# Kernel optimization log

Hardware: AMD Instinct MI355X
Metric: run time of the kernel (lower is better)

## Reference

```python
import jax, jax.numpy as jnp
import numpy as np

BETA = 100.0
# (in_ch, out_ch) for the 12 effective 1x1-conv layers. ResNeXt blocks are
# fused: all branches read the same block input, so stacking branch weights
# along out-channels gives one GEMM per block.
LAYER_DIMS = [(259, 515), (515, 512), (512, 512), (512, 576), (576, 576),
              (576, 768), (768, 768), (768, 768), (768, 960), (960, 960),
              (960, 896), (896, 1)]


def setup_inputs() -> dict:
    key = jax.random.key(0)
    keys = jax.random.split(key, 2 + len(LAYER_DIMS))
    B, N = 2, 8192
    inp = {
        "input": jax.random.normal(keys[0], (B, N, 3), dtype=jnp.float32),
        "latent": jax.random.normal(keys[1], (B, 256), dtype=jnp.float32),
    }
    for i, (cin, cout) in enumerate(LAYER_DIMS):
        std = np.sqrt(2.0) / np.sqrt(cin)
        inp[f"W{i+1}"] = std * jax.random.normal(keys[2 + i], (cout, cin), dtype=jnp.float32)
        inp[f"b{i+1}"] = jnp.zeros((cout,), dtype=jnp.float32)
    return inp


def _sp(z):
    # torch Softplus(beta=100): softplus(beta*z)/beta (jax.nn.softplus is stable)
    return jax.nn.softplus(BETA * z) / BETA


def reference(input, latent,
              W1, b1, W2, b2, W3, b3, W4, b4, W5, b5, W6, b6,
              W7, b7, W8, b8, W9, b9, W10, b10, W11, b11, W12, b12):
    B, N, _ = input.shape
    lat = jnp.broadcast_to(latent[:, None, :], (B, N, latent.shape[-1]))
    x = jnp.concatenate([input, lat], axis=-1)  # (B, N, 259)
    input_con = x

    # layer 1: conv + softplus, grad seeded from first 3 input columns (xyz)
    z = x @ W1.T + b1                                   # (B, N, 515)
    g = jax.nn.sigmoid(BETA * z)[..., None] * W1[:, :3]  # (B, N, 515, 3)
    x = _sp(z)

    mids = [(W2, b2), (W3, b3), (W4, b4), (W5, b5), (W6, b6), (W7, b7),
            (W8, b8), (W9, b9), (W10, b10), (W11, b11)]
    for W, b in mids:  # fixed small layer loop (10 fused ResNeXt blocks)
        z = x @ W.T + b                                 # (B, N, Cout)
        g = jax.nn.sigmoid(BETA * z)[..., None] * jnp.einsum('oc,bnci->bnoi', W, g)
        x = _sp(z)

    # final 1x1 conv, no activation
    z = x @ W12.T + b12                                 # (B, N, 1)
    g = jnp.einsum('oc,bnci->bnoi', W12, g)             # (B, N, 1, 3)
    # torch returns conv output channel-first: (B, 1, N)
    return (z.transpose(0, 2, 1), g, input_con)
```

## Files before the change

kernel.cpp:

```cpp
#include <hip/hip_runtime.h>
#include <math.h>


typedef unsigned short u16;
typedef _Float16 f16;
typedef f16   f16x8  __attribute__((ext_vector_type(8)));
typedef float f32x16 __attribute__((ext_vector_type(16)));

__device__ __forceinline__ u16   f2h(float x){ return __builtin_bit_cast(u16, (f16)x); }
__device__ __forceinline__ float h2f(u16 b){ return (float)__builtin_bit_cast(f16, b); }

__device__ __forceinline__ void glld16(const void* g, void* l){
  __builtin_amdgcn_global_load_lds(
      (const __attribute__((address_space(1))) unsigned*)g,
      (__attribute__((address_space(3))) unsigned*)l, 16, 0, 0);
}

template<int N> __device__ __forceinline__ void wait_vmcnt(){
  static_assert(N == 0 || N == 6 || N == 9, "unsupported vmcnt literal");
  if constexpr (N == 0) asm volatile("s_waitcnt vmcnt(0)" ::: "memory");
  if constexpr (N == 6) asm volatile("s_waitcnt vmcnt(6)" ::: "memory");
  if constexpr (N == 9) asm volatile("s_waitcnt vmcnt(9)" ::: "memory");
}

template<int NP>
__global__ __launch_bounds__(256, 2)
void fused_layer(const u16* __restrict__ Sin, long long psIn, int kpad,
                 u16* __restrict__ Sout, long long psOut, int opitch,
                 const u16* __restrict__ Wh, const u16* __restrict__ Wl,
                 const float* __restrict__ bias, const float* __restrict__ Wfirst,
                 int cout, int cinFirst)
{
  constexpr bool FIRST = (NP == 2);
  constexpr int  S     = NP + 4;
  __shared__ u16 As[2][NP][4][64][8];
  __shared__ u16 Bs[2][2][4][128][8];

  int bx = blockIdx.x, by = blockIdx.y;
  {
    const int gx = gridDim.x, gy = gridDim.y;
    const int nwg = gx * gy;
    const int d   = by * gx + bx;
    if ((nwg & 7) == 0){
      const int q = nwg >> 3;
      const int t = (d & 7) * q + (d >> 3);
      by = t % gy;
      bx = t / gy;
    }
  }

  const int tid   = threadIdx.x;
  const int w     = tid >> 6;
  const int lane  = tid & 63;
  const int lrow  = lane & 31;
  const int lhalf = lane >> 5;
  const int mh    = w >> 1;
  const int oh    = w & 1;
  const int m0    = bx * 64;
  const int o0    = by * 128;

  f32x16 zinit = {};
  f32x16 accx[2];
  f32x16 accg[FIRST ? 1 : 3][2];
  accx[0] = zinit; accx[1] = zinit;
  if constexpr (!FIRST){
    #pragma unroll
    for (int j = 0; j < 3; ++j){ accg[j][0] = zinit; accg[j][1] = zinit; }
  }

  const u16* aSrc[NP];
  #pragma unroll
  for (int p = 0; p < NP; ++p)
    aSrc[p] = Sin + (long long)p * psIn + (long long)(m0 + lane) * kpad + w * 8;
  const u16* bSrc[2][2];
  #pragma unroll
  for (int h = 0; h < 2; ++h){
    const u16* Wx = h ? Wl : Wh;
    #pragma unroll
    for (int hf = 0; hf < 2; ++hf)
      bSrc[h][hf] = Wx + (long long)(o0 + hf*64 + lane) * kpad + w * 8;
  }

  auto stage = [&](int buf, int kElem){
    #pragma unroll
    for (int p = 0; p < NP; ++p)
      glld16(aSrc[p] + kElem, &As[buf][p][w][0][0]);
    #pragma unroll
    for (int h = 0; h < 2; ++h)
      #pragma unroll
      for (int hf = 0; hf < 2; ++hf)
        glld16(bSrc[h][hf] + kElem, &Bs[buf][h][w][hf*64][0]);
  };

  auto compute = [&](int buf){
    __builtin_amdgcn_s_setprio(1);
    #pragma unroll
    for (int s = 0; s < 2; ++s){
      const int kq = s*2 + lhalf;
      f16x8 a[NP];
      #pragma unroll
      for (int p = 0; p < NP; ++p)
        a[p] = *(const f16x8*)&As[buf][p][kq][mh*32 + lrow][0];
      #pragma unroll
      for (int f = 0; f < 2; ++f){
        const int oc = oh*64 + f*32 + lrow;
        f16x8 bh = *(const f16x8*)&Bs[buf][0][kq][oc][0];
        f16x8 bl = *(const f16x8*)&Bs[buf][1][kq][oc][0];
        accx[f] = __builtin_amdgcn_mfma_f32_32x32x16_f16(a[0], bh, accx[f], 0,0,0);
        accx[f] = __builtin_amdgcn_mfma_f32_32x32x16_f16(a[1], bh, accx[f], 0,0,0);
        accx[f] = __builtin_amdgcn_mfma_f32_32x32x16_f16(a[0], bl, accx[f], 0,0,0);
        if constexpr (!FIRST){
          #pragma unroll
          for (int j = 0; j < 3; ++j)
            accg[j][f] = __builtin_amdgcn_mfma_f32_32x32x16_f16(a[2+j], bh, accg[j][f], 0,0,0);
        }
      }
    }
    __builtin_amdgcn_s_setprio(0);
  };

  const int nk = kpad >> 5;
  stage(0, 0);
  stage(1, 32);
  int cur = 0;
  for (int t = 0; t < nk - 1; ++t){
    wait_vmcnt<S>();
    __builtin_amdgcn_s_barrier();
    compute(cur);
    asm volatile("s_waitcnt lgkmcnt(0)" ::: "memory");
    __builtin_amdgcn_s_barrier();
    if (t + 2 < nk) stage(cur, (t + 2) * 32);
    cur ^= 1;
  }
  wait_vmcnt<0>();
  __builtin_amdgcn_s_barrier();
  compute(cur);

  const int mb = m0 + mh*32;
  #pragma unroll
  for (int f = 0; f < 2; ++f){
    const int o = o0 + oh*64 + f*32 + lrow;
    const float bo = (o < cout) ? bias[o] : 0.f;
    float w0 = 0.f, w1 = 0.f, w2 = 0.f;
    if constexpr (FIRST){
      if (o < cout){
        w0 = Wfirst[(long long)o*cinFirst + 0];
        w1 = Wfirst[(long long)o*cinFirst + 1];
        w2 = Wfirst[(long long)o*cinFirst + 2];
      }
    }
    #pragma unroll
    for (int r = 0; r < 16; ++r){
      const int m = mb + (r & 3) + ((r >> 2) << 3) + (lhalf << 2);
      const float z    = accx[f][r] + bo;
      const float gate = 1.f / (1.f + expf(-100.f * z));
      const float sp   = fmaxf(z, 0.f) + 0.01f * log1pf(expf(-100.f * fabsf(z)));
      const long long idx = (long long)m * opitch + o;
      const u16 xh = f2h(sp);
      Sout[idx]          = xh;
      Sout[psOut + idx]  = f2h(sp - h2f(xh));
      if constexpr (FIRST){
        Sout[2*psOut + idx] = f2h(gate * w0);
        Sout[3*psOut + idx] = f2h(gate * w1);
        Sout[4*psOut + idx] = f2h(gate * w2);
      } else {
        Sout[2*psOut + idx] = f2h(gate * accg[0][f][r]);
        Sout[3*psOut + idx] = f2h(gate * accg[1][f][r]);
        Sout[4*psOut + idx] = f2h(gate * accg[2][f][r]);
      }
    }
  }
}

__global__ __launch_bounds__(256)
void final_layer(const u16* __restrict__ Sin, long long ps, int kpad,
                 const float* __restrict__ W, const float* __restrict__ bias,
                 float* __restrict__ out1, float* __restrict__ out2,
                 int cin, int mBase)
{
  const int lane = threadIdx.x & 63;
  const int wv   = threadIdx.x >> 6;
  const int m = blockIdx.x * 4 + wv;
  const u16* row = Sin + (long long)m * kpad;
  float s0=0.f, s1=0.f, s2=0.f, s3=0.f;
  for (int c = lane; c < cin; c += 64){
    const float w = W[c];
    s0 += (h2f(row[c]) + h2f(row[ps + c])) * w;
    s1 += h2f(row[2*ps + c]) * w;
    s2 += h2f(row[3*ps + c]) * w;
    s3 += h2f(row[4*ps + c]) * w;
  }
  #pragma unroll
  for (int off = 32; off > 0; off >>= 1){
    s0 += __shfl_xor(s0, off); s1 += __shfl_xor(s1, off);
    s2 += __shfl_xor(s2, off); s3 += __shfl_xor(s3, off);
  }
  if (lane == 0){
    out1[mBase + m] = s0 + bias[0];
    float* g = out2 + (long long)(mBase + m) * 3;
    g[0] = s1; g[1] = s2; g[2] = s3;
  }
}

__global__ void prep_input(const float* __restrict__ input,
                           const float* __restrict__ latent,
                           float* __restrict__ out3,
                           u16* __restrict__ x0, long long psX0, int N)
{
  const int m = blockIdx.x;
  const int b = m / N;
  const int c = threadIdx.x;
  if (c >= 288) return;
  float v = 0.f;
  if (c < 3) v = input[(long long)m*3 + c];
  else if (c < 259) v = latent[(long long)b*256 + (c - 3)];
  if (c < 259) out3[(long long)m*259 + c] = v;
  const u16 h = f2h(v);
  x0[(long long)m*288 + c]        = h;
  x0[psX0 + (long long)m*288 + c] = f2h(v - h2f(h));
}

__global__ void split_w(const float* __restrict__ W, u16* __restrict__ wh,
                        u16* __restrict__ wl, int cout, int cin, int kpad, int total)
{
  const int idx = blockIdx.x * 256 + threadIdx.x;
  if (idx >= total) return;
  const int o = idx / kpad, c = idx % kpad;
  const float v = (o < cout && c < cin) ? W[(long long)o*cin + c] : 0.f;
  const u16 h = f2h(v);
  wh[idx] = h;
  wl[idx] = f2h(v - h2f(h));
}

extern "C" void kernel_launch(void* const* d_in, const int* in_sizes, int n_in,
                              void* d_out, int out_size, void* d_ws, size_t ws_size,
                              hipStream_t stream)
{
  static const int CIN [12] = {259,515,512,512,576,576,768,768,768,960,960,896};
  static const int COUT[12] = {515,512,512,576,576,768,768,768,960,960,896,1};
  int OPAD[11], KPAD[12];
  KPAD[0] = 288;
  for (int i = 0; i < 11; ++i){
    OPAD[i] = ((COUT[i] + 127) / 128) * 128;
    KPAD[i+1] = OPAD[i];
  }

  const float* input  = (const float*)d_in[0];
  const float* latent = (const float*)d_in[1];
  auto Wp = [&](int i){ return (const float*)d_in[2 + 2*i]; };
  auto Bp = [&](int i){ return (const float*)d_in[3 + 2*i]; };

  const int Bn = in_sizes[1] / 256;
  const int Nn = in_sizes[0] / (3 * Bn);
  const int M  = Bn * Nn;

  float* out1 = (float*)d_out;
  float* out2 = out1 + M;
  float* out3 = out2 + (size_t)M * 3;

  char* wsp = (char*)d_ws;
  u16 *WH[11], *WL[11];
  for (int i = 0; i < 11; ++i){
    const size_t sz = (size_t)OPAD[i] * KPAD[i] * 2;
    WH[i] = (u16*)wsp; wsp += sz;
    WL[i] = (u16*)wsp; wsp += sz;
  }
  u16* x0 = (u16*)wsp;
  const long long psX0 = (long long)M * 288;
  wsp += (size_t)2 * psX0 * 2;

  const size_t used = (size_t)(wsp - (char*)d_ws);
  const size_t remain = (ws_size > used) ? (ws_size - used) : 0;
  const size_t perPoint = (size_t)2 * 5 * 1024 * 2;
  long long pc = (long long)(remain / perPoint);
  pc &= ~63LL;
  int Pc = (int)((pc < 8192LL) ? pc : 8192LL);
  if (Pc > M) Pc = M;
  if (Pc < 64) Pc = 64;
  u16* bufA = (u16*)wsp;
  u16* bufB = bufA + (size_t)5 * Pc * 1024;

  prep_input<<<M, 320, 0, stream>>>(input, latent, out3, x0, psX0, Nn);
  for (int i = 0; i < 11; ++i){
    const int total = OPAD[i] * KPAD[i];
    split_w<<<(total + 255)/256, 256, 0, stream>>>(
        Wp(i), WH[i], WL[i], COUT[i], CIN[i], KPAD[i], total);
  }

  for (int cm0 = 0; cm0 < M; cm0 += Pc){
    const int Mc = (M - cm0 < Pc) ? (M - cm0) : Pc;

    {
      dim3 g(Mc/64, OPAD[0]/128);
      fused_layer<2><<<g, 256, 0, stream>>>(
          x0 + (long long)cm0 * 288, psX0, 288,
          bufA, (long long)Pc * OPAD[0], OPAD[0],
          WH[0], WL[0], Bp(0), Wp(0), COUT[0], CIN[0]);
    }
    u16* src = bufA;
    u16* dst = bufB;
    for (int i = 1; i <= 10; ++i){
      dim3 g(Mc/64, OPAD[i]/128);
      fused_layer<5><<<g, 256, 0, stream>>>(
          src, (long long)Pc * KPAD[i], KPAD[i],
          dst, (long long)Pc * OPAD[i], OPAD[i],
          WH[i], WL[i], Bp(i), nullptr, COUT[i], 0);
      u16* t = src; src = dst; dst = t;
    }
    final_layer<<<Mc/4, 256, 0, stream>>>(
        src, (long long)Pc * KPAD[11], KPAD[11],
        Wp(11), Bp(11), out1, out2, CIN[11], cm0);
  }
}
```

Measured before the change: 2.569 ms.

## Widen GEMM tile to 256 output channels with 8 waves and triple-buffered LDS

Each fused layer block now covers 64 points by 256 output channels using 512 threads (8 waves), so each staged A tile is reused across twice as many outputs. The load pipeline goes from double to triple buffering, with global->LDS chunks distributed evenly across waves and vmcnt waits computed per wave. Output channels are padded to 256, so some waves sit idle on layers whose width isn't a multiple of 256 (e.g. 515, 576, 896), and the larger LDS footprint may lower occupancy.

```diff
diff --git a/kernel.cpp b/kernel.cpp
--- a/kernel.cpp
+++ b/kernel.cpp
@@ -17,14 +17,18 @@
 }
 
 template<int N> __device__ __forceinline__ void wait_vmcnt(){
-  static_assert(N == 0 || N == 6 || N == 9, "unsupported vmcnt literal");
-  if constexpr (N == 0) asm volatile("s_waitcnt vmcnt(0)" ::: "memory");
-  if constexpr (N == 6) asm volatile("s_waitcnt vmcnt(6)" ::: "memory");
-  if constexpr (N == 9) asm volatile("s_waitcnt vmcnt(9)" ::: "memory");
+  static_assert(N==0||N==5||N==6||N==7||N==10||N==12||N==14, "bad vmcnt");
+  if constexpr (N == 0)  asm volatile("s_waitcnt vmcnt(0)"  ::: "memory");
+  if constexpr (N == 5)  asm volatile("s_waitcnt vmcnt(5)"  ::: "memory");
+  if constexpr (N == 6)  asm volatile("s_waitcnt vmcnt(6)"  ::: "memory");
+  if constexpr (N == 7)  asm volatile("s_waitcnt vmcnt(7)"  ::: "memory");
+  if constexpr (N == 10) asm volatile("s_waitcnt vmcnt(10)" ::: "memory");
+  if constexpr (N == 12) asm volatile("s_waitcnt vmcnt(12)" ::: "memory");
+  if constexpr (N == 14) asm volatile("s_waitcnt vmcnt(14)" ::: "memory");
 }
 
 template<int NP>
-__global__ __launch_bounds__(256, 2)
+__global__ __launch_bounds__(512, 2)
 void fused_layer(const u16* __restrict__ Sin, long long psIn, int kpad,
                  u16* __restrict__ Sout, long long psOut, int opitch,
                  const u16* __restrict__ Wh, const u16* __restrict__ Wl,
@@ -32,9 +36,15 @@
                  int cout, int cinFirst)
 {
   constexpr bool FIRST = (NP == 2);
-  constexpr int  S     = NP + 4;
-  __shared__ u16 As[2][NP][4][64][8];
-  __shared__ u16 Bs[2][2][4][128][8];
+  constexpr int ACH   = NP * 4;
+  constexpr int CH    = ACH + 32;
+  constexpr int ABUFE = NP * 2048;
+  constexpr int BUFE  = ABUFE + 16384;
+  constexpr int CBASE = CH / 8;
+  constexpr int CREM  = CH % 8;
+  constexpr int MAXC  = CBASE + (CREM ? 1 : 0);
+
+  __shared__ __align__(16) u16 lds[3 * BUFE];
 
   int bx = blockIdx.x, by = blockIdx.y;
   {
@@ -49,15 +59,37 @@
     }
   }
 
-  const int tid   = threadIdx.x;
-  const int w     = tid >> 6;
-  const int lane  = tid & 63;
-  const int lrow  = lane & 31;
-  const int lhalf = lane >> 5;
-  const int mh    = w >> 1;
-  const int oh    = w & 1;
-  const int m0    = bx * 64;
-  const int o0    = by * 128;
+  const int tid  = threadIdx.x;
+  const int ws   = __builtin_amdgcn_readfirstlane(tid >> 6);
+  const int lane = tid & 63;
+  const int lrow = lane & 31;
+  const int lhalf= lane >> 5;
+  const int mh   = ws & 1;
+  const int oq   = ws >> 1;
+  const int m0   = bx * 64;
+  const int o0   = by * 256;
+  const bool act = (o0 + oq * 64) < opitch;
+
+  const int cnt = (CREM && ws < CREM) ? CBASE + 1 : CBASE;
+  const int c0  = (CREM && ws < CREM) ? ws * (CBASE + 1)
+                                      : CREM * (CBASE + 1) + (ws - CREM) * CBASE;
+  const u16* gptr[MAXC];
+  int ldsOffE[MAXC];
+  #pragma unroll
+  for (int j = 0; j < MAXC; ++j){
+    const int c = c0 + ((j < cnt) ? j : 0);
+    if (c < ACH){
+      const int p = c >> 2, kq = c & 3;
+      gptr[j]    = Sin + (long long)p * psIn + (long long)m0 * kpad + kq * 8;
+      ldsOffE[j] = p * 2048 + kq * 512;
+    } else {
+      const int b = c - ACH;
+      const int h = b >> 4, kq = (b >> 2) & 3, gg = b & 3;
+      gptr[j]    = (h ? Wl : Wh) + (long long)(o0 + gg * 64) * kpad + kq * 8;
+      ldsOffE[j] = ABUFE + h * 8192 + kq * 2048 + gg * 512;
+    }
+  }
+  const int vLane = lane * kpad;
 
   f32x16 zinit = {};
   f32x16 accx[2];
@@ -68,44 +100,30 @@
     for (int j = 0; j < 3; ++j){ accg[j][0] = zinit; accg[j][1] = zinit; }
   }
 
-  const u16* aSrc[NP];
-  #pragma unroll
-  for (int p = 0; p < NP; ++p)
-    aSrc[p] = Sin + (long long)p * psIn + (long long)(m0 + lane) * kpad + w * 8;
-  const u16* bSrc[2][2];
-  #pragma unroll
-  for (int h = 0; h < 2; ++h){
-    const u16* Wx = h ? Wl : Wh;
+  auto stage = [&](int bufE, int ktE){
     #pragma unroll
-    for (int hf = 0; hf < 2; ++hf)
-      bSrc[h][hf] = Wx + (long long)(o0 + hf*64 + lane) * kpad + w * 8;
-  }
-
-  auto stage = [&](int buf, int kElem){
-    #pragma unroll
-    for (int p = 0; p < NP; ++p)
-      glld16(aSrc[p] + kElem, &As[buf][p][w][0][0]);
-    #pragma unroll
-    for (int h = 0; h < 2; ++h)
-      #pragma unroll
-      for (int hf = 0; hf < 2; ++hf)
-        glld16(bSrc[h][hf] + kElem, &Bs[buf][h][w][hf*64][0]);
+    for (int j = 0; j < MAXC; ++j)
+      if (j < cnt)
+        glld16(gptr[j] + vLane + ktE, &lds[bufE + ldsOffE[j]]);
   };
 
-  auto compute = [&](int buf){
+  auto compute = [&](int bufE){
+    if (!act) return;
     __builtin_amdgcn_s_setprio(1);
     #pragma unroll
     for (int s = 0; s < 2; ++s){
-      const int kq = s*2 + lhalf;
+      const int kq = s * 2 + lhalf;
+      const int aoff = bufE + kq * 512 + (mh * 32 + lrow) * 8;
       f16x8 a[NP];
       #pragma unroll
       for (int p = 0; p < NP; ++p)
-        a[p] = *(const f16x8*)&As[buf][p][kq][mh*32 + lrow][0];
+        a[p] = *(const f16x8*)&lds[aoff + p * 2048];
       #pragma unroll
       for (int f = 0; f < 2; ++f){
-        const int oc = oh*64 + f*32 + lrow;
-        f16x8 bh = *(const f16x8*)&Bs[buf][0][kq][oc][0];
-        f16x8 bl = *(const f16x8*)&Bs[buf][1][kq][oc][0];
+        const int row  = oq * 64 + f * 32 + lrow;
+        const int boff = bufE + ABUFE + kq * 2048 + row * 8;
+        f16x8 bh = *(const f16x8*)&lds[boff];
+        f16x8 bl = *(const f16x8*)&lds[boff + 8192];
         accx[f] = __builtin_amdgcn_mfma_f32_32x32x16_f16(a[0], bh, accx[f], 0,0,0);
         accx[f] = __builtin_amdgcn_mfma_f32_32x32x16_f16(a[1], bh, accx[f], 0,0,0);
         accx[f] = __builtin_amdgcn_mfma_f32_32x32x16_f16(a[0], bl, accx[f], 0,0,0);
@@ -121,32 +139,40 @@
 
   const int nk = kpad >> 5;
   stage(0, 0);
-  stage(1, 32);
-  int cur = 0;
-  for (int t = 0; t < nk - 1; ++t){
-    wait_vmcnt<S>();
+  stage(BUFE, 32);
+  stage(2 * BUFE, 64);
+  int bufE = 0;
+  for (int t = 0; t < nk; ++t){
+    const int ahead = nk - 1 - t;
+    if (ahead >= 2){
+      if (CREM && cnt == CBASE + 1) wait_vmcnt<2*CBASE + 2>();
+      else                          wait_vmcnt<2*CBASE>();
+    } else if (ahead == 1){
+      if (CREM && cnt == CBASE + 1) wait_vmcnt<CBASE + 1>();
+      else                          wait_vmcnt<CBASE>();
+    } else {
+      wait_vmcnt<0>();
+    }
     __builtin_amdgcn_s_barrier();
-    compute(cur);
+    compute(bufE);
     asm volatile("s_waitcnt lgkmcnt(0)" ::: "memory");
     __builtin_amdgcn_s_barrier();
-    if (t + 2 < nk) stage(cur, (t + 2) * 32);
-    cur ^= 1;
-  }
-  wait_vmcnt<0>();
-  __builtin_amdgcn_s_barrier();
-  compute(cur);
-
-  const int mb = m0 + mh*32;
+    if (t + 3 < nk) stage(bufE, (t + 3) * 32);
+    bufE += BUFE; if (bufE == 3 * BUFE) bufE = 0;
+  }
+
+  if (!act) return;
+  const int mb = m0 + mh * 32;
   #pragma unroll
   for (int f = 0; f < 2; ++f){
-    const int o = o0 + oh*64 + f*32 + lrow;
+    const int o = o0 + oq * 64 + f * 32 + lrow;
     const float bo = (o < cout) ? bias[o] : 0.f;
     float w0 = 0.f, w1 = 0.f, w2 = 0.f;
     if constexpr (FIRST){
       if (o < cout){
-        w0 = Wfirst[(long long)o*cinFirst + 0];
-        w1 = Wfirst[(long long)o*cinFirst + 1];
-        w2 = Wfirst[(long long)o*cinFirst + 2];
+        w0 = Wfirst[(long long)o * cinFirst + 0];
+        w1 = Wfirst[(long long)o * cinFirst + 1];
+        w2 = Wfirst[(long long)o * cinFirst + 2];
       }
     }
     #pragma unroll
@@ -238,10 +264,11 @@
 {
   static const int CIN [12] = {259,515,512,512,576,576,768,768,768,960,960,896};
   static const int COUT[12] = {515,512,512,576,576,768,768,768,960,960,896,1};
-  int OPAD[11], KPAD[12];
+  int OPAD[11], OP256[11], KPAD[12];
   KPAD[0] = 288;
   for (int i = 0; i < 11; ++i){
-    OPAD[i] = ((COUT[i] + 127) / 128) * 128;
+    OPAD[i]  = ((COUT[i] + 127) / 128) * 128;
+    OP256[i] = ((COUT[i] + 255) / 256) * 256;
     KPAD[i+1] = OPAD[i];
   }
 
@@ -261,7 +288,7 @@
   char* wsp = (char*)d_ws;
   u16 *WH[11], *WL[11];
   for (int i = 0; i < 11; ++i){
-    const size_t sz = (size_t)OPAD[i] * KPAD[i] * 2;
+    const size_t sz = (size_t)OP256[i] * KPAD[i] * 2;
     WH[i] = (u16*)wsp; wsp += sz;
     WL[i] = (u16*)wsp; wsp += sz;
   }
@@ -282,7 +309,7 @@
 
   prep_input<<<M, 320, 0, stream>>>(input, latent, out3, x0, psX0, Nn);
   for (int i = 0; i < 11; ++i){
-    const int total = OPAD[i] * KPAD[i];
+    const int total = OP256[i] * KPAD[i];
     split_w<<<(total + 255)/256, 256, 0, stream>>>(
         Wp(i), WH[i], WL[i], COUT[i], CIN[i], KPAD[i], total);
   }
@@ -291,8 +318,8 @@
     const int Mc = (M - cm0 < Pc) ? (M - cm0) : Pc;
 
     {
-      dim3 g(Mc/64, OPAD[0]/128);
-      fused_layer<2><<<g, 256, 0, stream>>>(
+      dim3 g(Mc/64, OP256[0]/256);
+      fused_layer<2><<<g, 512, 0, stream>>>(
           x0 + (long long)cm0 * 288, psX0, 288,
           bufA, (long long)Pc * OPAD[0], OPAD[0],
           WH[0], WL[0], Bp(0), Wp(0), COUT[0], CIN[0]);
@@ -300,8 +327,8 @@
     u16* src = bufA;
     u16* dst = bufB;
     for (int i = 1; i <= 10; ++i){
-      dim3 g(Mc/64, OPAD[i]/128);
-      fused_layer<5><<<g, 256, 0, stream>>>(
+      dim3 g(Mc/64, OP256[i]/256);
+      fused_layer<5><<<g, 512, 0, stream>>>(
           src, (long long)Pc * KPAD[i], KPAD[i],
           dst, (long long)Pc * OPAD[i], OPAD[i],
           WH[i], WL[i], Bp(i), nullptr, COUT[i], 0);
```

After: 3.313 ms. 28.9% more time.
